# Kernel tuning notes

Hardware: AMD Instinct MI355X
Metric: run time of the kernel (lower is better)

Reference implementation:

```python
import jax, jax.numpy as jnp
import numpy as np

B, CIN, C, N, K = 2, 64, 128, 8192, 16
GROUPS = C // 16
EPS = 1e-5


def lrelu(x):
    return jnp.where(x >= 0, x, 0.1 * x)


def conv1d(x, w, b):  # x:(B,Ci,N) w:(Co,Ci)
    return jnp.einsum('oc,bcn->bon', w, x) + b[None, :, None]


def conv2d(x, w, b):  # x:(B,Ci,N,K) w:(Co,Ci)
    return jnp.einsum('oc,bcnk->bonk', w, x) + b[None, :, None, None]


def groupnorm(x, gamma, beta, groups=GROUPS):
    # normalize over (C/groups, *spatial) per sample per group
    b, c = x.shape[0], x.shape[1]
    xr = x.reshape(b, groups, -1)
    mean = xr.mean(-1, keepdims=True)
    var = xr.var(-1, keepdims=True)
    xn = ((xr - mean) * jax.lax.rsqrt(var + EPS)).reshape(x.shape)
    shp = (1, c) + (1,) * (x.ndim - 2)
    return xn * gamma.reshape(shp) + beta.reshape(shp)


def knn_idx(xyz, k):  # xyz:(B,3,N) -> idx:(B,N,K)
    pts = jnp.transpose(xyz, (0, 2, 1))  # (B,N,3)
    sq = jnp.sum(pts * pts, axis=-1)  # (B,N)
    inner = jnp.einsum('bnc,bmc->bnm', pts, pts)
    d2 = sq[:, :, None] + sq[:, None, :] - 2.0 * inner  # (B,N,N)
    _, idx = jax.lax.top_k(-d2, k)
    return idx


def group(x, idx):  # x:(B,C,N) idx:(B,N,K) -> (B,C,N,K)
    b, c, n = x.shape
    k = idx.shape[-1]
    idxe = jnp.broadcast_to(idx.reshape(b, 1, n * k), (b, c, n * k))
    return jnp.take_along_axis(x, idxe, axis=2).reshape(b, c, n, k)


def reference(xyz, feat, pre_w, pre_b, wq_w, wq_b, wk_w, wk_b, wv_w, wv_b,
              pos1_w, pos1_b, pos1_g, pos1_be, pos2_w, pos2_b,
              att1_w, att1_b, att1_g, att1_be, att2_w, att2_b,
              post_w, post_b, post_g, post_be):
    idx = knn_idx(xyz, K)  # (B,N,K)
    new_feat = conv1d(feat, pre_w, pre_b)  # (B,C,N)
    rel = group(xyz, idx) - xyz[:, :, :, None]  # (B,3,N,K)
    pos = lrelu(groupnorm(conv2d(rel, pos1_w, pos1_b), pos1_g, pos1_be))
    pos = conv2d(pos, pos2_w, pos2_b)  # (B,C,N,K)
    q = conv1d(new_feat, wq_w, wq_b)
    k = group(conv1d(new_feat, wk_w, wk_b), idx)  # (B,C,N,K)
    v = group(conv1d(new_feat, wv_w, wv_b), idx)
    att = q[:, :, :, None] - k + pos
    att = lrelu(groupnorm(conv2d(att, att1_w, att1_b), att1_g, att1_be))
    att = conv2d(att, att2_w, att2_b)
    att = jax.nn.softmax(att, axis=3)
    out = jnp.sum(att * v, axis=3)  # (B,C,N)
    out = lrelu(groupnorm(conv1d(out + new_feat, post_w, post_b), post_g, post_be))
    return out


def setup_inputs():
    key = jax.random.key(0)
    ks = jax.random.split(key, 16)
    s = 0.05
    d = {
        'xyz': jax.random.normal(ks[0], (B, 3, N), jnp.float32),
        'feat': jax.random.normal(ks[1], (B, CIN, N), jnp.float32),
        'pre_w': jax.random.normal(ks[2], (C, CIN), jnp.float32) * s,
        'pre_b': jnp.zeros((C,), jnp.float32),
        'wq_w': jax.random.normal(ks[3], (C, C), jnp.float32) * s,
        'wq_b': jnp.zeros((C,), jnp.float32),
        'wk_w': jax.random.normal(ks[4], (C, C), jnp.float32) * s,
        'wk_b': jnp.zeros((C,), jnp.float32),
        'wv_w': jax.random.normal(ks[5], (C, C), jnp.float32) * s,
        'wv_b': jnp.zeros((C,), jnp.float32),
        'pos1_w': jax.random.normal(ks[6], (C, 3), jnp.float32) * s,
        'pos1_b': jnp.zeros((C,), jnp.float32),
        'pos1_g': jnp.ones((C,), jnp.float32),
        'pos1_be': jnp.zeros((C,), jnp.float32),
        'pos2_w': jax.random.normal(ks[7], (C, C), jnp.float32) * s,
        'pos2_b': jnp.zeros((C,), jnp.float32),
        'att1_w': jax.random.normal(ks[8], (C, C), jnp.float32) * s,
        'att1_b': jnp.zeros((C,), jnp.float32),
        'att1_g': jnp.ones((C,), jnp.float32),
        'att1_be': jnp.zeros((C,), jnp.float32),
        'att2_w': jax.random.normal(ks[9], (C, C), jnp.float32) * s,
        'att2_b': jnp.zeros((C,), jnp.float32),
        'post_w': jax.random.normal(ks[10], (C, C), jnp.float32) * s,
        'post_b': jnp.zeros((C,), jnp.float32),
        'post_g': jnp.ones((C,), jnp.float32),
        'post_be': jnp.zeros((C,), jnp.float32),
    }
    return d
```

## Files before the change

### kernel.cpp

```cpp
#include <hip/hip_runtime.h>
#include <hip/hip_bf16.h>

#define BB 2
#define NN 8192
#define CC 128
#define CIN_ 64
#define KK 16
#define EPSV 1e-5f

typedef __attribute__((ext_vector_type(8))) short short8;
typedef __attribute__((ext_vector_type(4))) float f32x4;

static const size_t OFF_NF   = 262144;
static const size_t OFF_OUT2 = OFF_NF  + 2097152;
static const size_t OFF_Y    = OFF_OUT2 + 2097152;
static const size_t OFF_AQB  = OFF_Y   + 16777216;
static const size_t OFF_AKB  = OFF_AQB + 1048576;
static const size_t OFF_VFB  = OFF_AKB + 1048576;
static const size_t OFF_WQ2  = OFF_VFB + 1048576;
static const size_t OFF_WK2  = OFF_WQ2 + 16384;
static const size_t OFF_PWT  = OFF_WK2 + 16384;
static const size_t OFF_W2B  = OFF_PWT + 16384;
static const size_t OFF_A2B  = OFF_W2B + 8192;
static const size_t OFF_BY   = OFF_A2B + 8192;
static const size_t OFF_RST  = OFF_BY  + 128;
static const size_t OFF_REDA = OFF_RST + 32;
static const size_t OFF_REDP = OFF_REDA + 32;
static const size_t OFF_S1   = OFF_REDP + 32;
static const size_t OFF_T1   = OFF_S1 + 256;
static const size_t OFF_S2   = OFF_T1 + 256;
static const size_t OFF_T2   = OFF_S2 + 256;
static const size_t OFF_S3   = OFF_T2 + 256;
static const size_t OFF_T3   = OFF_S3 + 256;
static const size_t OFF_PTS4 = OFF_T3 + 256;
static const size_t OFF_PTA  = OFF_PTS4 + 65536;
static const size_t OFF_PTP  = OFF_PTA + 65536;

__device__ __forceinline__ unsigned fkey_u(float d) {
  unsigned u = __float_as_uint(d);
  return (u & 0x80000000u) ? ~u : (u | 0x80000000u);
}
__device__ __forceinline__ unsigned long long shflx64(unsigned long long v, int m) {
  int lo = __shfl_xor((int)(unsigned)(v & 0xffffffffu), m, 64);
  int hi = __shfl_xor((int)(unsigned)(v >> 32), m, 64);
  return ((unsigned long long)(unsigned)hi << 32) | (unsigned)lo;
}
__device__ __forceinline__ float bf2f(unsigned short u) {
  return __uint_as_float((unsigned)u << 16);
}
__device__ __forceinline__ unsigned short f2bf(float f) {
  __hip_bfloat16 h = __float2bfloat16(f);
  unsigned short r;
  __builtin_memcpy(&r, &h, 2);
  return r;
}
__device__ __forceinline__ unsigned pack2bf(float a, float b) {
  return (unsigned)f2bf(a) | ((unsigned)f2bf(b) << 16);
}

__global__ __launch_bounds__(128) void prep_weights(
    const float* __restrict__ att1_w, const float* __restrict__ wq_w, const float* __restrict__ wk_w,
    const float* __restrict__ pos2_w, const float* __restrict__ att2_w, const float* __restrict__ post_w,
    const float* __restrict__ wq_b, const float* __restrict__ wk_b, const float* __restrict__ pos2_b,
    const float* __restrict__ att1_b,
    float* __restrict__ WQ2, float* __restrict__ WK2, __hip_bfloat16* __restrict__ W2b,
    __hip_bfloat16* __restrict__ A2b, float* __restrict__ PWT, float* __restrict__ bias_y) {
  int blk = blockIdx.x, t = threadIdx.x;
  if (blk < 128) {
    int c = blk;
    __shared__ float row[128];
    row[t] = att1_w[c * 128 + t];
    __syncthreads();
    float sq = 0.f, sk = 0.f, sp = 0.f;
    for (int m = 0; m < 128; ++m) {
      float r = row[m];
      sq = fmaf(r, wq_w[m * 128 + t], sq);
      sk = fmaf(r, wk_w[m * 128 + t], sk);
      sp = fmaf(r, pos2_w[m * 128 + t], sp);
    }
    WQ2[c * 128 + t] = sq;
    WK2[c * 128 + t] = sk;
    W2b[c * 128 + t] = __float2bfloat16(sp);
  } else if (blk == 128) {
    for (int e = t; e < 16384; e += 128) {
      int c = e >> 7, cp = e & 127;
      A2b[e] = __float2bfloat16(att2_w[e]);
      PWT[cp * 128 + c] = post_w[e];
    }
  } else {
    float s = att1_b[t];
    for (int m = 0; m < 128; ++m)
      s = fmaf(att1_w[t * 128 + m], wq_b[m] - wk_b[m] + pos2_b[m], s);
    bias_y[t] = s;
  }
}

__global__ __launch_bounds__(256) void pts4_kernel(const float* __restrict__ xyz,
                                                   float4* __restrict__ pts4) {
  int e = blockIdx.x * 256 + threadIdx.x;
  int b = e >> 13, n = e & 8191;
  const float* X = xyz + b * 3 * NN;
  float x = X[n], y = X[NN + n], z = X[2 * NN + n];
  pts4[e] = make_float4(-2.0f * x, -2.0f * y, -2.0f * z, fmaf(z, z, fmaf(y, y, x * x)));
}

#define SLOTS 96
__global__ __launch_bounds__(512) void knn_kernel(const float4* __restrict__ pts4,
                                                  int* __restrict__ idxb) {
  __shared__ unsigned long long list[16][SLOTS];
  __shared__ float chm[16][33];
  __shared__ float taus[16];
  __shared__ int cnt[16];
  int t = threadIdx.x;
  int wid = t >> 6, lane = t & 63;
  int blk = blockIdx.x;
  int b = blk >> 9;
  int q0 = (blk & 511) << 4;
  const float4* P = pts4 + b * NN;
  if (t < 16) cnt[t] = 0;
  float qx[16], qy[16], qz[16];
#pragma unroll
  for (int j = 0; j < 16; ++j) {
    float4 qv = P[q0 + j];
    qx[j] = -0.5f * qv.x; qy[j] = -0.5f * qv.y; qz[j] = -0.5f * qv.z;
  }

  {
    int g = lane >> 4, s = lane & 15;
    const float4* Pc = P + (wid << 10) + (g << 8);
    float mn[16];
#pragma unroll
    for (int j = 0; j < 16; ++j) mn[j] = 3.4e38f;
    for (int i = 0; i < 16; i += 2) {
      float4 c0 = Pc[(i << 4) + s];
      float4 c1 = Pc[((i + 1) << 4) + s];
#pragma unroll
      for (int j = 0; j < 16; ++j) {
        float d0 = fmaf(qx[j], c0.x, fmaf(qy[j], c0.y, fmaf(qz[j], c0.z, c0.w)));
        float d1 = fmaf(qx[j], c1.x, fmaf(qy[j], c1.y, fmaf(qz[j], c1.z, c1.w)));
        mn[j] = fminf(mn[j], fminf(d0, d1));
      }
    }
#pragma unroll
    for (int off = 1; off < 16; off <<= 1)
#pragma unroll
      for (int j = 0; j < 16; ++j) mn[j] = fminf(mn[j], __shfl_xor(mn[j], off));
    if (s == 0) {
#pragma unroll
      for (int j = 0; j < 16; ++j) chm[j][(wid << 2) + g] = mn[j];
    }
  }
  __syncthreads();

  if (t < 16) {
    float v[32];
#pragma unroll
    for (int i = 0; i < 32; ++i) v[i] = chm[t][i];
    float lo = v[0], hi = v[0];
#pragma unroll
    for (int i = 1; i < 32; ++i) { lo = fminf(lo, v[i]); hi = fmaxf(hi, v[i]); }
    for (int it = 0; it < 12; ++it) {
      float mid = 0.5f * (lo + hi);
      int c = 0;
#pragma unroll
      for (int i = 0; i < 32; ++i) c += (v[i] <= mid) ? 1 : 0;
      if (c >= 16) hi = mid; else lo = mid;
    }
    taus[t] = hi;
  }
  __syncthreads();
  float tauv[16];
#pragma unroll
  for (int j = 0; j < 16; ++j) tauv[j] = taus[j];

  for (int i = 0; i < 16; ++i) {
    int ci = (wid << 10) + (i << 6) + lane;
    float4 cv = P[ci];
#pragma unroll
    for (int j = 0; j < 16; ++j) {
      float d = fmaf(qx[j], cv.x, fmaf(qy[j], cv.y, fmaf(qz[j], cv.z, cv.w)));
      if (d <= tauv[j]) {
        int sl = atomicAdd(&cnt[j], 1);
        if (sl < SLOTS)
          list[j][sl] = ((unsigned long long)fkey_u(d) << 32) | (unsigned)ci;
      }
    }
  }
  __syncthreads();

  {
    int qa = wid << 1, qb2 = qa + 1;
    int ca = cnt[qa]; if (ca > SLOTS) ca = SLOTS;
    int cb3 = cnt[qb2]; if (cb3 > SLOTS) cb3 = SLOTS;
    unsigned long long k0a = (lane < ca) ? list[qa][lane] : ~0ULL;
    unsigned long long k1a = (lane + 64 < ca) ? list[qa][lane + 64] : ~0ULL;
    unsigned long long k0b = (lane < cb3) ? list[qb2][lane] : ~0ULL;
    unsigned long long k1b = (lane + 64 < cb3) ? list[qb2][lane + 64] : ~0ULL;
    for (int r = 0; r < 16; ++r) {
      unsigned long long wa = (k0a < k1a) ? k0a : k1a;
      unsigned long long wb = (k0b < k1b) ? k0b : k1b;
      for (int off = 32; off; off >>= 1) {
        unsigned long long oa = shflx64(wa, off);
        unsigned long long ob = shflx64(wb, off);
        if (oa < wa) wa = oa;
        if (ob < wb) wb = ob;
      }
      if (k0a == wa) k0a = ~0ULL; else if (k1a == wa) k1a = ~0ULL;
      if (k0b == wb) k0b = ~0ULL; else if (k1b == wb) k1b = ~0ULL;
      if (lane == 0) {
        idxb[((size_t)(b * NN) + q0 + qa) * 16 + r] = (int)(wa & 0xffffffffu);
        idxb[((size_t)(b * NN) + q0 + qb2) * 16 + r] = (int)(wb & 0xffffffffu);
      }
    }
  }
}

__global__ __launch_bounds__(256) void relstats_kernel(const float* __restrict__ xyz,
                                                       const int* __restrict__ idxb,
                                                       float* __restrict__ rst) {
  int b = blockIdx.x >> 8;
  int nbase = (blockIdx.x & 255) << 5;
  const float* X = xyz + b * 3 * NN;
  float a[9];
#pragma unroll
  for (int m = 0; m < 9; ++m) a[m] = 0.f;
  for (int e = threadIdx.x; e < 512; e += 256) {
    int nn = nbase + (e >> 4);
    int kk = e & 15;
    int j = idxb[(b * NN + nn) * 16 + kk];
    float rx = X[j] - X[nn];
    float ry = X[NN + j] - X[NN + nn];
    float rz = X[2 * NN + j] - X[2 * NN + nn];
    a[0] += rx; a[1] += ry; a[2] += rz;
    a[3] = fmaf(rx, rx, a[3]); a[4] = fmaf(rx, ry, a[4]); a[5] = fmaf(rx, rz, a[5]);
    a[6] = fmaf(ry, ry, a[6]); a[7] = fmaf(ry, rz, a[7]); a[8] = fmaf(rz, rz, a[8]);
  }
  __shared__ float red[4][9];
  int lane = threadIdx.x & 63, wid = threadIdx.x >> 6;
#pragma unroll
  for (int m = 0; m < 9; ++m) {
    float v = a[m];
    for (int off = 32; off; off >>= 1) v += __shfl_xor(v, off, 64);
    if (lane == 0) red[wid][m] = v;
  }
  __syncthreads();
  if (threadIdx.x < 9) {
    float v = red[0][threadIdx.x] + red[1][threadIdx.x] + red[2][threadIdx.x] + red[3][threadIdx.x];
    atomicAdd(&rst[b * 16 + threadIdx.x], v);
  }
}

__global__ __launch_bounds__(256) void t1_kernel(const float* __restrict__ rst,
    const float* __restrict__ pos1_w, const float* __restrict__ pos1_b,
    const float* __restrict__ pos1_g, const float* __restrict__ pos1_be,
    float* __restrict__ s1, float* __restrict__ t1) {
  __shared__ float gsum[16], gsum2[16];
  int t = threadIdx.x;
  if (t < 16) { gsum[t] = 0.f; gsum2[t] = 0.f; }
  __syncthreads();
  int b = t >> 7, c = t & 127;
  const float* S = rst + b * 16;
  const float Minv = 1.0f / (float)(NN * KK);
  float mx = S[0] * Minv, my = S[1] * Minv, mz = S[2] * Minv;
  float Mxx = S[3] * Minv, Mxy = S[4] * Minv, Mxz = S[5] * Minv;
  float Myy = S[6] * Minv, Myz = S[7] * Minv, Mzz = S[8] * Minv;
  float w0 = pos1_w[c * 3], w1 = pos1_w[c * 3 + 1], w2 = pos1_w[c * 3 + 2];
  float bb = pos1_b[c];
  float wm = w0 * mx + w1 * my + w2 * mz;
  float Ey = wm + bb;
  float q = w0 * w0 * Mxx + w1 * w1 * Myy + w2 * w2 * Mzz
          + 2.f * (w0 * w1 * Mxy + w0 * w2 * Mxz + w1 * w2 * Myz);
  float Ey2 = q + 2.f * bb * wm + bb * bb;
  int g = c >> 4;
  atomicAdd(&gsum[b * 8 + g], Ey);
  atomicAdd(&gsum2[b * 8 + g], Ey2);
  __syncthreads();
  float mean = gsum[b * 8 + g] * (1.f / 16.f);
  float var = fmaxf(gsum2[b * 8 + g] * (1.f / 16.f) - mean * mean, 0.f);
  float r = rsqrtf(var + EPSV);
  float sv = pos1_g[c] * r;
  s1[t] = sv;
  t1[t] = fmaf(sv, bb, pos1_be[c] - mean * sv);
}

__global__ __launch_bounds__(256) void feat_kernel(
    const float* __restrict__ feat, const float* __restrict__ pre_w, const float* __restrict__ pre_b,
    const float* __restrict__ WQ2, const float* __restrict__ WK2,
    const float* __restrict__ wv_w, const float* __restrict__ wv_b,
    float* __restrict__ nf, __hip_bfloat16* __restrict__ AqTb,
    __hip_bfloat16* __restrict__ AkTb, __hip_bfloat16* __restrict__ vfTb) {
  int b = blockIdx.x >> 9;
  int n0 = (blockIdx.x & 511) << 4;
  __shared__ float fe[64][20];
  __shared__ float nfs[128][20];
  int t = threadIdx.x;
  for (int e = t; e < 1024; e += 256) {
    int ci = e >> 4, nn2 = e & 15;
    fe[ci][nn2] = feat[(b * 64 + ci) * NN + n0 + nn2];
  }
  __syncthreads();
  int nq = t & 3, cw = t >> 2;
  {
    float acc[2][4];
#pragma unroll
    for (int m = 0; m < 2; ++m) {
      float bv = pre_b[cw + 64 * m];
      acc[m][0] = bv; acc[m][1] = bv; acc[m][2] = bv; acc[m][3] = bv;
    }
    for (int i = 0; i < 64; ++i) {
      float4 x = *(const float4*)&fe[i][nq << 2];
      float w0 = pre_w[cw * 64 + i];
      float w1 = pre_w[(cw + 64) * 64 + i];
      acc[0][0] = fmaf(w0, x.x, acc[0][0]); acc[0][1] = fmaf(w0, x.y, acc[0][1]);
      acc[0][2] = fmaf(w0, x.z, acc[0][2]); acc[0][3] = fmaf(w0, x.w, acc[0][3]);
      acc[1][0] = fmaf(w1, x.x, acc[1][0]); acc[1][1] = fmaf(w1, x.y, acc[1][1]);
      acc[1][2] = fmaf(w1, x.z, acc[1][2]); acc[1][3] = fmaf(w1, x.w, acc[1][3]);
    }
#pragma unroll
    for (int m = 0; m < 2; ++m) {
      int c = cw + 64 * m;
      float4 v = make_float4(acc[m][0], acc[m][1], acc[m][2], acc[m][3]);
      *(float4*)&nfs[c][nq << 2] = v;
      *(float4*)&nf[(b * 128 + c) * NN + n0 + (nq << 2)] = v;
    }
  }
  __syncthreads();
  for (int s = 0; s < 3; ++s) {
    const float* Wm = (s == 0) ? WQ2 : ((s == 1) ? WK2 : wv_w);
    __hip_bfloat16* D = (s == 0) ? AqTb : ((s == 1) ? AkTb : vfTb);
    float acc[2][4];
#pragma unroll
    for (int m = 0; m < 2; ++m) {
      float bv = (s == 2) ? wv_b[cw + 64 * m] : 0.f;
      acc[m][0] = bv; acc[m][1] = bv; acc[m][2] = bv; acc[m][3] = bv;
    }
    for (int i = 0; i < 128; ++i) {
      float4 x = *(const float4*)&nfs[i][nq << 2];
      float w0 = Wm[cw * 128 + i];
      float w1 = Wm[(cw + 64) * 128 + i];
      acc[0][0] = fmaf(w0, x.x, acc[0][0]); acc[0][1] = fmaf(w0, x.y, acc[0][1]);
      acc[0][2] = fmaf(w0, x.z, acc[0][2]); acc[0][3] = fmaf(w0, x.w, acc[0][3]);
      acc[1][0] = fmaf(w1, x.x, acc[1][0]); acc[1][1] = fmaf(w1, x.y, acc[1][1]);
      acc[1][2] = fmaf(w1, x.z, acc[1][2]); acc[1][3] = fmaf(w1, x.w, acc[1][3]);
    }
#pragma unroll
    for (int m = 0; m < 2; ++m) {
      int c = cw + 64 * m;
#pragma unroll
      for (int v = 0; v < 4; ++v)
        D[(size_t)(b * NN + n0 + (nq << 2) + v) * 128 + c] = __float2bfloat16(acc[m][v]);
    }
  }
}

__global__ __launch_bounds__(256) void y_kernel_mfma(const float* __restrict__ xyz,
    const int* __restrict__ idxb, const __hip_bfloat16* __restrict__ AqTb,
    const __hip_bfloat16* __restrict__ AkTb, const __hip_bfloat16* __restrict__ W2b,
    const float* __restrict__ bias_y, const float* __restrict__ pos1_w,
    const float* __restrict__ s1, const float* __restrict__ t1,
    __hip_bfloat16* __restrict__ ybuf, float* __restrict__ partA) {
  int b = blockIdx.x >> 11;
  int pb = (blockIdx.x & 2047) * 4;
  __shared__ __align__(16) __hip_bfloat16 z_s[64][136];
  __shared__ __align__(16) __hip_bfloat16 ak_s[64][136];
  __shared__ __align__(16) float aq_s[4][128];
  __shared__ float rel_s[64][4];
  __shared__ int jj[64];
  __shared__ float gns[8], gns2[8];
  int t = threadIdx.x;
  int lane = t & 63, wid = t >> 6;
  int l15 = lane & 15, quad = lane >> 4;
  if (t < 8) { gns[t] = 0.f; gns2[t] = 0.f; }
  if (t < 64) {
    int n = pb + (t >> 4);
    int j = idxb[(b * NN + pb) * 16 + t];
    jj[t] = j;
    const float* X = xyz + b * 3 * NN;
    rel_s[t][0] = X[j] - X[n];
    rel_s[t][1] = X[NN + j] - X[NN + n];
    rel_s[t][2] = X[2 * NN + j] - X[2 * NN + n];
  }
  for (int e = t; e < 512; e += 256) {
    int pt = e >> 7, c = e & 127;
    aq_s[pt][c] = bf2f(((const unsigned short*)AqTb)[((size_t)(b * NN) + pb + pt) * 128 + c]) + bias_y[c];
  }
  __syncthreads();
  {
    int cpp = t & 63, pg = t >> 6;
    int cp0 = cpp * 2;
    float w00 = pos1_w[cp0 * 3], w01 = pos1_w[cp0 * 3 + 1], w02 = pos1_w[cp0 * 3 + 2];
    float w10 = pos1_w[cp0 * 3 + 3], w11 = pos1_w[cp0 * 3 + 4], w12 = pos1_w[cp0 * 3 + 5];
    float sa = s1[b * 128 + cp0], ta = t1[b * 128 + cp0];
    float sb = s1[b * 128 + cp0 + 1], tb = t1[b * 128 + cp0 + 1];
#pragma unroll
    for (int i = 0; i < 16; ++i) {
      int pix = pg * 16 + i;
      float rx = rel_s[pix][0], ry = rel_s[pix][1], rz = rel_s[pix][2];
      float u0 = fmaf(w02, rz, fmaf(w01, ry, w00 * rx));
      float u1 = fmaf(w12, rz, fmaf(w11, ry, w10 * rx));
      float z0 = fmaf(sa, u0, ta); z0 = (z0 >= 0.f) ? z0 : 0.1f * z0;
      float z1 = fmaf(sb, u1, tb); z1 = (z1 >= 0.f) ? z1 : 0.1f * z1;
      *(unsigned*)&z_s[pix][cp0] = pack2bf(z0, z1);
    }
  }
  for (int e = t; e < 4096; e += 256) {
    int pix = e >> 6, cpp = e & 63;
    *(unsigned*)&ak_s[pix][cpp * 2] =
        *(const unsigned*)((const unsigned short*)AkTb + ((size_t)(b * NN) + jj[pix]) * 128 + cpp * 2);
  }
  short8 afr[2][4];
#pragma unroll
  for (int m2 = 0; m2 < 2; ++m2) {
    int row = (wid * 2 + m2) * 16 + l15;
#pragma unroll
    for (int k0 = 0; k0 < 4; ++k0)
      afr[m2][k0] = *(const short8*)((const unsigned short*)W2b + row * 128 + k0 * 32 + quad * 8);
  }
  __syncthreads();
  f32x4 acc[2][4];
#pragma unroll
  for (int m2 = 0; m2 < 2; ++m2)
#pragma unroll
    for (int nt = 0; nt < 4; ++nt) acc[m2][nt] = (f32x4){0.f, 0.f, 0.f, 0.f};
#pragma unroll
  for (int k0 = 0; k0 < 4; ++k0) {
#pragma unroll
    for (int nt = 0; nt < 4; ++nt) {
      short8 bfr = *(const short8*)&z_s[nt * 16 + l15][k0 * 32 + quad * 8];
      acc[0][nt] = __builtin_amdgcn_mfma_f32_16x16x32_bf16(afr[0][k0], bfr, acc[0][nt], 0, 0, 0);
      acc[1][nt] = __builtin_amdgcn_mfma_f32_16x16x32_bf16(afr[1][k0], bfr, acc[1][nt], 0, 0, 0);
    }
  }
  float lsum[2] = {0.f, 0.f}, lsum2[2] = {0.f, 0.f};
#pragma unroll
  for (int m2 = 0; m2 < 2; ++m2) {
    int c0 = (wid * 2 + m2) * 16 + quad * 4;
#pragma unroll
    for (int nt = 0; nt < 4; ++nt) {
      int pix = nt * 16 + l15;
      ushort4 au = *(ushort4*)&ak_s[pix][c0];
      float4 aq = *(float4*)&aq_s[nt][c0];
      f32x4 a = acc[m2][nt];
      float v0 = a[0] + aq.x - bf2f(au.x);
      float v1 = a[1] + aq.y - bf2f(au.y);
      float v2 = a[2] + aq.z - bf2f(au.z);
      float v3 = a[3] + aq.w - bf2f(au.w);
      lsum[m2] += (v0 + v1) + (v2 + v3);
      lsum2[m2] += fmaf(v0, v0, fmaf(v1, v1, fmaf(v2, v2, v3 * v3)));
      ushort4 yo;
      yo.x = f2bf(v0); yo.y = f2bf(v1); yo.z = f2bf(v2); yo.w = f2bf(v3);
      *(ushort4*)&ak_s[pix][c0] = yo;
    }
  }
#pragma unroll
  for (int m2 = 0; m2 < 2; ++m2) {
    float s = lsum[m2], s2 = lsum2[m2];
    for (int msk = 1; msk < 64; msk <<= 1) {
      s += __shfl_xor(s, msk);
      s2 += __shfl_xor(s2, msk);
    }
    if (lane == 0) {
      atomicAdd(&gns[wid * 2 + m2], s);
      atomicAdd(&gns2[wid * 2 + m2], s2);
    }
  }
  __syncthreads();
  size_t ybase = ((size_t)(b * NN) + pb) * 16;
  unsigned short* yb = (unsigned short*)ybuf;
  for (int e = t; e < 4096; e += 256) {
    int pix = e >> 6, cpp = e & 63;
    *(unsigned*)(yb + (ybase + pix) * 128 + cpp * 2) = *(unsigned*)&ak_s[pix][cpp * 2];
  }
  if (t < 8) {
    partA[(size_t)t * 4096 + blockIdx.x] = gns[t];
    partA[(size_t)(8 + t) * 4096 + blockIdx.x] = gns2[t];
  }
}

__global__ __launch_bounds__(256) void gnred_kernel(const float* __restrict__ part,
                                                    float* __restrict__ red) {
  int k = blockIdx.x;
  int pb = k >> 4, idx = k & 15;
  const float* p = part + (size_t)idx * 4096 + pb * 2048;
  float s = 0.f;
  for (int i = threadIdx.x; i < 2048; i += 256) s += p[i];
  __shared__ float rs[4];
  int lane = threadIdx.x & 63, wid = threadIdx.x >> 6;
  for (int off = 32; off; off >>= 1) s += __shfl_xor(s, off);
  if (lane == 0) rs[wid] = s;
  __syncthreads();
  if (threadIdx.x == 0) red[k] = rs[0] + rs[1] + rs[2] + rs[3];
}

__global__ __launch_bounds__(256) void att_out_kernel(const __hip_bfloat16* __restrict__ ybuf,
    const int* __restrict__ idxb, const float* __restrict__ redA,
    const float* __restrict__ att1_g, const float* __restrict__ att1_be,
    const __hip_bfloat16* __restrict__ A2b, const __hip_bfloat16* __restrict__ vfTb,
    const float* __restrict__ nf, const float* __restrict__ PWT, const float* __restrict__ post_b,
    float* __restrict__ out2, float* __restrict__ partP) {
  int b = blockIdx.x >> 11;
  int pb = (blockIdx.x & 2047) * 4;
  __shared__ __align__(16) union HS {
    unsigned short h[64][136];
    float sc[2][128][17];
  } hs;
  __shared__ __align__(16) __hip_bfloat16 v_s[64][136];
  __shared__ __align__(16) float opre[4][132];
  __shared__ int jj[64];
  __shared__ float gns[8], gns2[8];
  int t = threadIdx.x;
  int lane = t & 63, wid = t >> 6;
  int l15 = lane & 15, quad = lane >> 4;
  if (t < 8) { gns[t] = 0.f; gns2[t] = 0.f; }
  if (t < 64) jj[t] = idxb[(b * NN + pb) * 16 + t];
  __syncthreads();
  size_t ybase = ((size_t)(b * NN) + pb) * 16;
  const unsigned short* yb = (const unsigned short*)ybuf;
  {
    int cpp = t & 63, pg = t >> 6;
    int c0 = cpp * 2;
    const float Minv = 1.0f / 2097152.0f;
    int g = c0 >> 4;
    float S = redA[b * 16 + g], S2v = redA[b * 16 + 8 + g];
    float mean = S * Minv;
    float var = fmaxf(S2v * Minv - mean * mean, 0.f);
    float r = rsqrtf(var + EPSV);
    float sa = att1_g[c0] * r;
    float ta = att1_be[c0] - mean * sa;
    float sb = att1_g[c0 + 1] * r;
    float tb = att1_be[c0 + 1] - mean * sb;
#pragma unroll
    for (int i = 0; i < 16; ++i) {
      int pix = pg * 16 + i;
      unsigned u = *(const unsigned*)(yb + (ybase + pix) * 128 + c0);
      float y0 = bf2f((unsigned short)(u & 0xffff));
      float y1 = bf2f((unsigned short)(u >> 16));
      float h0 = fmaf(sa, y0, ta); h0 = (h0 >= 0.f) ? h0 : 0.1f * h0;
      float h1 = fmaf(sb, y1, tb); h1 = (h1 >= 0.f) ? h1 : 0.1f * h1;
      *(unsigned*)&hs.h[pix][c0] = pack2bf(h0, h1);
    }
  }
  for (int e = t; e < 4096; e += 256) {
    int pix = e >> 6, cpp = e & 63;
    *(unsigned*)&v_s[pix][cpp * 2] =
        *(const unsigned*)((const unsigned short*)vfTb + ((size_t)(b * NN) + jj[pix]) * 128 + cpp * 2);
  }
  short8 afr[2][4];
#pragma unroll
  for (int m2 = 0; m2 < 2; ++m2) {
    int row = (wid * 2 + m2) * 16 + l15;
#pragma unroll
    for (int k0 = 0; k0 < 4; ++k0)
      afr[m2][k0] = *(const short8*)((const unsigned short*)A2b + row * 128 + k0 * 32 + quad * 8);
  }
  __syncthreads();
  f32x4 acc[2][4];
#pragma unroll
  for (int m2 = 0; m2 < 2; ++m2)
#pragma unroll
    for (int nt = 0; nt < 4; ++nt) acc[m2][nt] = (f32x4){0.f, 0.f, 0.f, 0.f};
#pragma unroll
  for (int k0 = 0; k0 < 4; ++k0) {
#pragma unroll
    for (int nt = 0; nt < 4; ++nt) {
      short8 bfr = *(const short8*)&hs.h[nt * 16 + l15][k0 * 32 + quad * 8];
      acc[0][nt] = __builtin_amdgcn_mfma_f32_16x16x32_bf16(afr[0][k0], bfr, acc[0][nt], 0, 0, 0);
      acc[1][nt] = __builtin_amdgcn_mfma_f32_16x16x32_bf16(afr[1][k0], bfr, acc[1][nt], 0, 0, 0);
    }
  }
  int pidx = t >> 7;
  int cch = t & 127;
#pragma unroll
  for (int pass = 0; pass < 2; ++pass) {
    __syncthreads();
#pragma unroll
    for (int ntl = 0; ntl < 2; ++ntl) {
      int nt = pass * 2 + ntl;
#pragma unroll
      for (int m2 = 0; m2 < 2; ++m2) {
        int cb = (wid * 2 + m2) * 16 + quad * 4;
        f32x4 a = acc[m2][nt];
#pragma unroll
        for (int r = 0; r < 4; ++r) hs.sc[ntl][cb + r][l15] = a[r];
      }
    }
    __syncthreads();
    {
      int p = pass * 2 + pidx;
      float nfv = nf[(size_t)(b * 128 + cch) * NN + pb + p];
      const float* srow = hs.sc[pidx][cch];
      float sv[16];
#pragma unroll
      for (int k = 0; k < 16; ++k) sv[k] = srow[k];
      float mx = sv[0];
#pragma unroll
      for (int k = 1; k < 16; ++k) mx = fmaxf(mx, sv[k]);
      float sm = 0.f, dot = 0.f;
#pragma unroll
      for (int k = 0; k < 16; ++k) {
        float e = __expf(sv[k] - mx);
        sm += e;
        float vv = bf2f(*(const unsigned short*)&v_s[p * 16 + k][cch]);
        dot = fmaf(e, vv, dot);
      }
      opre[p][cch] = dot / sm + nfv;
    }
  }
  __syncthreads();
  {
    int c = t & 127, g = t >> 7;
    float a0 = post_b[c], a1 = a0;
    for (int cp = 0; cp < 128; ++cp) {
      float w = PWT[cp * 128 + c];
      a0 = fmaf(w, opre[g * 2][cp], a0);
      a1 = fmaf(w, opre[g * 2 + 1][cp], a1);
    }
    out2[(size_t)(b * 128 + c) * NN + pb + g * 2] = a0;
    out2[(size_t)(b * 128 + c) * NN + pb + g * 2 + 1] = a1;
    atomicAdd(&gns[c >> 4], a0 + a1);
    atomicAdd(&gns2[c >> 4], fmaf(a0, a0, a1 * a1));
  }
  __syncthreads();
  if (t < 8) {
    partP[(size_t)t * 4096 + blockIdx.x] = gns[t];
    partP[(size_t)(8 + t) * 4096 + blockIdx.x] = gns2[t];
  }
}

__global__ __launch_bounds__(256) void final_kernel(const float* __restrict__ out2,
    const float* __restrict__ redP, const float* __restrict__ post_g,
    const float* __restrict__ post_be, float* __restrict__ out) {
  int e = blockIdx.x * 256 + threadIdx.x;
  int c = (e >> 13) & 127, b = e >> 20;
  const float Minv = 1.0f / 131072.0f;
  int g = c >> 4;
  float S = redP[b * 16 + g], S2 = redP[b * 16 + 8 + g];
  float mean = S * Minv;
  float var = fmaxf(S2 * Minv - mean * mean, 0.f);
  float r = rsqrtf(var + EPSV);
  float sv = post_g[c] * r;
  float tv = post_be[c] - mean * sv;
  float v = fmaf(sv, out2[e], tv);
  out[e] = (v >= 0.f) ? v : 0.1f * v;
}

extern "C" void kernel_launch(void* const* d_in, const int* in_sizes, int n_in,
                              void* d_out, int out_size, void* d_ws, size_t ws_size,
                              hipStream_t stream) {
  (void)in_sizes; (void)n_in; (void)out_size; (void)ws_size;
  const float* xyz     = (const float*)d_in[0];
  const float* feat    = (const float*)d_in[1];
  const float* pre_w   = (const float*)d_in[2];
  const float* pre_b   = (const float*)d_in[3];
  const float* wq_w    = (const float*)d_in[4];
  const float* wq_b    = (const float*)d_in[5];
  const float* wk_w    = (const float*)d_in[6];
  const float* wk_b    = (const float*)d_in[7];
  const float* wv_w    = (const float*)d_in[8];
  const float* wv_b    = (const float*)d_in[9];
  const float* pos1_w  = (const float*)d_in[10];
  const float* pos1_b  = (const float*)d_in[11];
  const float* pos1_g  = (const float*)d_in[12];
  const float* pos1_be = (const float*)d_in[13];
  const float* pos2_w  = (const float*)d_in[14];
  const float* pos2_b  = (const float*)d_in[15];
  const float* att1_w  = (const float*)d_in[16];
  const float* att1_b  = (const float*)d_in[17];
  const float* att1_g  = (const float*)d_in[18];
  const float* att1_be = (const float*)d_in[19];
  const float* att2_w  = (const float*)d_in[20];
  const float* post_w  = (const float*)d_in[22];
  const float* post_b  = (const float*)d_in[23];
  const float* post_g  = (const float*)d_in[24];
  const float* post_be = (const float*)d_in[25];

  float* W = (float*)d_ws;
  int* idxb = (int*)d_ws;
  float* nf   = W + OFF_NF;
  float* out2 = W + OFF_OUT2;
  __hip_bfloat16* ybuf = (__hip_bfloat16*)(W + OFF_Y);
  __hip_bfloat16* AqTb = (__hip_bfloat16*)(W + OFF_AQB);
  __hip_bfloat16* AkTb = (__hip_bfloat16*)(W + OFF_AKB);
  __hip_bfloat16* vfTb = (__hip_bfloat16*)(W + OFF_VFB);
  float* WQ2  = W + OFF_WQ2;
  float* WK2  = W + OFF_WK2;
  float* PWT  = W + OFF_PWT;
  __hip_bfloat16* W2b = (__hip_bfloat16*)(W + OFF_W2B);
  __hip_bfloat16* A2b = (__hip_bfloat16*)(W + OFF_A2B);
  float* BY   = W + OFF_BY;
  float* RST  = W + OFF_RST;
  float* REDA = W + OFF_REDA;
  float* REDP = W + OFF_REDP;
  float* S1 = W + OFF_S1; float* T1 = W + OFF_T1;
  float4* PTS4 = (float4*)(W + OFF_PTS4);
  float* PARTA = W + OFF_PTA;
  float* PARTP = W + OFF_PTP;

  hipMemsetAsync(RST, 0, 32 * sizeof(float), stream);

  prep_weights<<<130, 128, 0, stream>>>(att1_w, wq_w, wk_w, pos2_w, att2_w, post_w,
                                        wq_b, wk_b, pos2_b, att1_b,
                                        WQ2, WK2, W2b, A2b, PWT, BY);
  pts4_kernel<<<64, 256, 0, stream>>>(xyz, PTS4);
  knn_kernel<<<1024, 512, 0, stream>>>(PTS4, idxb);
  relstats_kernel<<<512, 256, 0, stream>>>(xyz, idxb, RST);
  t1_kernel<<<1, 256, 0, stream>>>(RST, pos1_w, pos1_b, pos1_g, pos1_be, S1, T1);
  feat_kernel<<<1024, 256, 0, stream>>>(feat, pre_w, pre_b, WQ2, WK2, wv_w, wv_b,
                                        nf, AqTb, AkTb, vfTb);
  y_kernel_mfma<<<4096, 256, 0, stream>>>(xyz, idxb, AqTb, AkTb, W2b, BY, pos1_w, S1, T1, ybuf, PARTA);
  gnred_kernel<<<32, 256, 0, stream>>>(PARTA, REDA);
  att_out_kernel<<<4096, 256, 0, stream>>>(ybuf, idxb, REDA, att1_g, att1_be,
                                           A2b, vfTb, nf, PWT, post_b, out2, PARTP);
  gnred_kernel<<<32, 256, 0, stream>>>(PARTP, REDP);
  final_kernel<<<8192, 256, 0, stream>>>(out2, REDP, post_g, post_be, (float*)d_out);
}
```

Before: 383.0 us.

## Halve knn block size, vectorize gathers, and read post_w rows directly

```diff
diff --git a/kernel.cpp b/kernel.cpp
--- a/kernel.cpp
+++ b/kernel.cpp
@@ -60,11 +60,11 @@
 
 __global__ __launch_bounds__(128) void prep_weights(
     const float* __restrict__ att1_w, const float* __restrict__ wq_w, const float* __restrict__ wk_w,
-    const float* __restrict__ pos2_w, const float* __restrict__ att2_w, const float* __restrict__ post_w,
+    const float* __restrict__ pos2_w, const float* __restrict__ att2_w,
     const float* __restrict__ wq_b, const float* __restrict__ wk_b, const float* __restrict__ pos2_b,
     const float* __restrict__ att1_b,
     float* __restrict__ WQ2, float* __restrict__ WK2, __hip_bfloat16* __restrict__ W2b,
-    __hip_bfloat16* __restrict__ A2b, float* __restrict__ PWT, float* __restrict__ bias_y) {
+    __hip_bfloat16* __restrict__ A2b, float* __restrict__ bias_y) {
   int blk = blockIdx.x, t = threadIdx.x;
   if (blk < 128) {
     int c = blk;
@@ -82,11 +82,8 @@
     WK2[c * 128 + t] = sk;
     W2b[c * 128 + t] = __float2bfloat16(sp);
   } else if (blk == 128) {
-    for (int e = t; e < 16384; e += 128) {
-      int c = e >> 7, cp = e & 127;
+    for (int e = t; e < 16384; e += 128)
       A2b[e] = __float2bfloat16(att2_w[e]);
-      PWT[cp * 128 + c] = post_w[e];
-    }
   } else {
     float s = att1_b[t];
     for (int m = 0; m < 128; ++m)
@@ -105,7 +102,7 @@
 }
 
 #define SLOTS 96
-__global__ __launch_bounds__(512) void knn_kernel(const float4* __restrict__ pts4,
+__global__ __launch_bounds__(256) void knn_kernel(const float4* __restrict__ pts4,
                                                   int* __restrict__ idxb) {
   __shared__ unsigned long long list[16][SLOTS];
   __shared__ float chm[16][33];
@@ -126,14 +123,14 @@
   }
 
   {
-    int g = lane >> 4, s = lane & 15;
-    const float4* Pc = P + (wid << 10) + (g << 8);
+    int g = lane >> 3, s = lane & 7;
+    const float4* Pc = P + (wid << 11) + (g << 8);
     float mn[16];
 #pragma unroll
     for (int j = 0; j < 16; ++j) mn[j] = 3.4e38f;
-    for (int i = 0; i < 16; i += 2) {
-      float4 c0 = Pc[(i << 4) + s];
-      float4 c1 = Pc[((i + 1) << 4) + s];
+    for (int i = 0; i < 32; i += 2) {
+      float4 c0 = Pc[(i << 3) + s];
+      float4 c1 = Pc[((i + 1) << 3) + s];
 #pragma unroll
       for (int j = 0; j < 16; ++j) {
         float d0 = fmaf(qx[j], c0.x, fmaf(qy[j], c0.y, fmaf(qz[j], c0.z, c0.w)));
@@ -142,12 +139,12 @@
       }
     }
 #pragma unroll
-    for (int off = 1; off < 16; off <<= 1)
+    for (int off = 1; off < 8; off <<= 1)
 #pragma unroll
       for (int j = 0; j < 16; ++j) mn[j] = fminf(mn[j], __shfl_xor(mn[j], off));
     if (s == 0) {
 #pragma unroll
-      for (int j = 0; j < 16; ++j) chm[j][(wid << 2) + g] = mn[j];
+      for (int j = 0; j < 16; ++j) chm[j][(wid << 3) + g] = mn[j];
     }
   }
   __syncthreads();
@@ -173,8 +170,8 @@
 #pragma unroll
   for (int j = 0; j < 16; ++j) tauv[j] = taus[j];
 
-  for (int i = 0; i < 16; ++i) {
-    int ci = (wid << 10) + (i << 6) + lane;
+  for (int i = 0; i < 32; ++i) {
+    int ci = (wid << 11) + (i << 6) + lane;
     float4 cv = P[ci];
 #pragma unroll
     for (int j = 0; j < 16; ++j) {
@@ -188,8 +185,8 @@
   }
   __syncthreads();
 
-  {
-    int qa = wid << 1, qb2 = qa + 1;
+  for (int pp = 0; pp < 2; ++pp) {
+    int qa = (wid << 2) + pp * 2, qb2 = qa + 1;
     int ca = cnt[qa]; if (ca > SLOTS) ca = SLOTS;
     int cb3 = cnt[qb2]; if (cb3 > SLOTS) cb3 = SLOTS;
     unsigned long long k0a = (lane < ca) ? list[qa][lane] : ~0ULL;
@@ -403,10 +400,10 @@
       *(unsigned*)&z_s[pix][cp0] = pack2bf(z0, z1);
     }
   }
-  for (int e = t; e < 4096; e += 256) {
-    int pix = e >> 6, cpp = e & 63;
-    *(unsigned*)&ak_s[pix][cpp * 2] =
-        *(const unsigned*)((const unsigned short*)AkTb + ((size_t)(b * NN) + jj[pix]) * 128 + cpp * 2);
+  for (int e = t; e < 1024; e += 256) {
+    int pix = e >> 4, q4 = e & 15;
+    *(float4*)&ak_s[pix][q4 * 8] =
+        *(const float4*)((const unsigned short*)AkTb + ((size_t)(b * NN) + jj[pix]) * 128 + q4 * 8);
   }
   short8 afr[2][4];
 #pragma unroll
@@ -467,9 +464,9 @@
   __syncthreads();
   size_t ybase = ((size_t)(b * NN) + pb) * 16;
   unsigned short* yb = (unsigned short*)ybuf;
-  for (int e = t; e < 4096; e += 256) {
-    int pix = e >> 6, cpp = e & 63;
-    *(unsigned*)(yb + (ybase + pix) * 128 + cpp * 2) = *(unsigned*)&ak_s[pix][cpp * 2];
+  for (int e = t; e < 1024; e += 256) {
+    int pix = e >> 4, q4 = e & 15;
+    *(float4*)(yb + (ybase + pix) * 128 + q4 * 8) = *(const float4*)&ak_s[pix][q4 * 8];
   }
   if (t < 8) {
     partA[(size_t)t * 4096 + blockIdx.x] = gns[t];
@@ -496,7 +493,7 @@
     const int* __restrict__ idxb, const float* __restrict__ redA,
     const float* __restrict__ att1_g, const float* __restrict__ att1_be,
     const __hip_bfloat16* __restrict__ A2b, const __hip_bfloat16* __restrict__ vfTb,
-    const float* __restrict__ nf, const float* __restrict__ PWT, const float* __restrict__ post_b,
+    const float* __restrict__ nf, const float* __restrict__ post_w, const float* __restrict__ post_b,
     float* __restrict__ out2, float* __restrict__ partP) {
   int b = blockIdx.x >> 11;
   int pb = (blockIdx.x & 2047) * 4;
@@ -517,33 +514,42 @@
   size_t ybase = ((size_t)(b * NN) + pb) * 16;
   const unsigned short* yb = (const unsigned short*)ybuf;
   {
-    int cpp = t & 63, pg = t >> 6;
-    int c0 = cpp * 2;
+    int c0 = (t & 15) * 8;
+    int pg = t >> 4;
     const float Minv = 1.0f / 2097152.0f;
     int g = c0 >> 4;
     float S = redA[b * 16 + g], S2v = redA[b * 16 + 8 + g];
     float mean = S * Minv;
     float var = fmaxf(S2v * Minv - mean * mean, 0.f);
     float r = rsqrtf(var + EPSV);
-    float sa = att1_g[c0] * r;
-    float ta = att1_be[c0] - mean * sa;
-    float sb = att1_g[c0 + 1] * r;
-    float tb = att1_be[c0 + 1] - mean * sb;
-#pragma unroll
-    for (int i = 0; i < 16; ++i) {
-      int pix = pg * 16 + i;
-      unsigned u = *(const unsigned*)(yb + (ybase + pix) * 128 + c0);
-      float y0 = bf2f((unsigned short)(u & 0xffff));
-      float y1 = bf2f((unsigned short)(u >> 16));
-      float h0 = fmaf(sa, y0, ta); h0 = (h0 >= 0.f) ? h0 : 0.1f * h0;
-      float h1 = fmaf(sb, y1, tb); h1 = (h1 >= 0.f) ? h1 : 0.1f * h1;
-      *(unsigned*)&hs.h[pix][c0] = pack2bf(h0, h1);
-    }
-  }
-  for (int e = t; e < 4096; e += 256) {
-    int pix = e >> 6, cpp = e & 63;
-    *(unsigned*)&v_s[pix][cpp * 2] =
-        *(const unsigned*)((const unsigned short*)vfTb + ((size_t)(b * NN) + jj[pix]) * 128 + cpp * 2);
+    float sarr[8], tarr[8];
+#pragma unroll
+    for (int u = 0; u < 8; ++u) {
+      sarr[u] = att1_g[c0 + u] * r;
+      tarr[u] = att1_be[c0 + u] - mean * sarr[u];
+    }
+#pragma unroll
+    for (int i = 0; i < 4; ++i) {
+      int pix = pg * 4 + i;
+      short8 yv = *(const short8*)(yb + (ybase + pix) * 128 + c0);
+      unsigned ww[4];
+#pragma unroll
+      for (int u = 0; u < 4; ++u) {
+        float y0 = bf2f((unsigned short)yv[u * 2]);
+        float y1 = bf2f((unsigned short)yv[u * 2 + 1]);
+        float h0 = fmaf(sarr[u * 2], y0, tarr[u * 2]);
+        h0 = (h0 >= 0.f) ? h0 : 0.1f * h0;
+        float h1 = fmaf(sarr[u * 2 + 1], y1, tarr[u * 2 + 1]);
+        h1 = (h1 >= 0.f) ? h1 : 0.1f * h1;
+        ww[u] = pack2bf(h0, h1);
+      }
+      *(float4*)&hs.h[pix][c0] = *(const float4*)ww;
+    }
+  }
+  for (int e = t; e < 1024; e += 256) {
+    int pix = e >> 4, q4 = e & 15;
+    *(float4*)&v_s[pix][q4 * 8] =
+        *(const float4*)((const unsigned short*)vfTb + ((size_t)(b * NN) + jj[pix]) * 128 + q4 * 8);
   }
   short8 afr[2][4];
 #pragma unroll
@@ -609,11 +615,15 @@
   __syncthreads();
   {
     int c = t & 127, g = t >> 7;
+    const float4* PW = (const float4*)(post_w + (size_t)c * 128);
     float a0 = post_b[c], a1 = a0;
-    for (int cp = 0; cp < 128; ++cp) {
-      float w = PWT[cp * 128 + c];
-      a0 = fmaf(w, opre[g * 2][cp], a0);
-      a1 = fmaf(w, opre[g * 2 + 1][cp], a1);
+    for (int cp4 = 0; cp4 < 32; ++cp4) {
+      float4 w = PW[cp4];
+      int cp = cp4 * 4;
+      a0 = fmaf(w.x, opre[g * 2][cp], a0);     a1 = fmaf(w.x, opre[g * 2 + 1][cp], a1);
+      a0 = fmaf(w.y, opre[g * 2][cp + 1], a0); a1 = fmaf(w.y, opre[g * 2 + 1][cp + 1], a1);
+      a0 = fmaf(w.z, opre[g * 2][cp + 2], a0); a1 = fmaf(w.z, opre[g * 2 + 1][cp + 2], a1);
+      a0 = fmaf(w.w, opre[g * 2][cp + 3], a0); a1 = fmaf(w.w, opre[g * 2 + 1][cp + 3], a1);
     }
     out2[(size_t)(b * 128 + c) * NN + pb + g * 2] = a0;
     out2[(size_t)(b * 128 + c) * NN + pb + g * 2 + 1] = a1;
@@ -684,7 +694,6 @@
   __hip_bfloat16* vfTb = (__hip_bfloat16*)(W + OFF_VFB);
   float* WQ2  = W + OFF_WQ2;
   float* WK2  = W + OFF_WK2;
-  float* PWT  = W + OFF_PWT;
   __hip_bfloat16* W2b = (__hip_bfloat16*)(W + OFF_W2B);
   __hip_bfloat16* A2b = (__hip_bfloat16*)(W + OFF_A2B);
   float* BY   = W + OFF_BY;
@@ -698,11 +707,11 @@
 
   hipMemsetAsync(RST, 0, 32 * sizeof(float), stream);
 
-  prep_weights<<<130, 128, 0, stream>>>(att1_w, wq_w, wk_w, pos2_w, att2_w, post_w,
+  prep_weights<<<130, 128, 0, stream>>>(att1_w, wq_w, wk_w, pos2_w, att2_w,
                                         wq_b, wk_b, pos2_b, att1_b,
-                                        WQ2, WK2, W2b, A2b, PWT, BY);
+                                        WQ2, WK2, W2b, A2b, BY);
   pts4_kernel<<<64, 256, 0, stream>>>(xyz, PTS4);
-  knn_kernel<<<1024, 512, 0, stream>>>(PTS4, idxb);
+  knn_kernel<<<1024, 256, 0, stream>>>(PTS4, idxb);
   relstats_kernel<<<512, 256, 0, stream>>>(xyz, idxb, RST);
   t1_kernel<<<1, 256, 0, stream>>>(RST, pos1_w, pos1_b, pos1_g, pos1_be, S1, T1);
   feat_kernel<<<1024, 256, 0, stream>>>(feat, pre_w, pre_b, WQ2, WK2, wv_w, wv_b,
@@ -710,7 +719,7 @@
   y_kernel_mfma<<<4096, 256, 0, stream>>>(xyz, idxb, AqTb, AkTb, W2b, BY, pos1_w, S1, T1, ybuf, PARTA);
   gnred_kernel<<<32, 256, 0, stream>>>(PARTA, REDA);
   att_out_kernel<<<4096, 256, 0, stream>>>(ybuf, idxb, REDA, att1_g, att1_be,
-                                           A2b, vfTb, nf, PWT, post_b, out2, PARTP);
+                                           A2b, vfTb, nf, post_w, post_b, out2, PARTP);
   gnred_kernel<<<32, 256, 0, stream>>>(PARTP, REDP);
   final_kernel<<<8192, 256, 0, stream>>>(out2, REDP, post_g, post_be, (float*)d_out);
 }
```

Measured after the change: 398.2 us. 1.04x slower.
